# Kernel optimization log

Measured on AMD Instinct MI355X. Metric: run time of the kernel, lower is better.

Reference implementation:

```python
import jax, jax.numpy as jnp
import numpy as np

B, S, D = 32, 4096, 256


def setup_inputs() -> dict:
    key = jax.random.key(0)
    kx, km = jax.random.split(key)
    x = jax.random.normal(kx, (B, S, D), dtype=jnp.float32)
    # keep_mask[b, t] == 1 means timestep t is kept (original: 1 - bernoulli(skipping_probs))
    keep_mask = jax.random.randint(km, (B, S), 0, 2, dtype=jnp.int32)
    return {"x": x, "keep_mask": keep_mask}


def reference(x, keep_mask):
    # Batched stream-compaction: move kept timesteps to the front of each row
    # (stable, preserving original order), zero-pad the tail.
    keep = keep_mask.astype(bool)                       # [B, S]
    # stable argsort of (not keep): kept indices first, in original time order
    order = jnp.argsort(jnp.logical_not(keep), axis=1, stable=True)  # [B, S]
    gathered = jnp.take_along_axis(x, order[:, :, None], axis=1)      # [B, S, D]
    counts = jnp.sum(keep, axis=1, keepdims=True)       # [B, 1] kept lengths
    valid = jnp.arange(S)[None, :] < counts             # [B, S]
    return gathered * valid[:, :, None].astype(x.dtype)
```

## Files before the change

kernel.cpp:

```cpp
#include <hip/hip_runtime.h>

constexpr int S_LEN = 4096;
constexpr int D_DIM = 256;

__global__ void scan_kernel(const int* __restrict__ mask,
                            int* __restrict__ pos,
                            int* __restrict__ counts) {
    const int b = blockIdx.x;
    __shared__ int wsum[8];
    const int tid = threadIdx.x;
    const int base = b * S_LEN + tid * 8;

    int4 m0 = *reinterpret_cast<const int4*>(mask + base);
    int4 m1 = *reinterpret_cast<const int4*>(mask + base + 4);
    int vals[8] = {m0.x, m0.y, m0.z, m0.w, m1.x, m1.y, m1.z, m1.w};

    int local = 0;
#pragma unroll
    for (int i = 0; i < 8; ++i) local += vals[i];

    const int lane = tid & 63;
    const int wid  = tid >> 6;

    int scan = local;
#pragma unroll
    for (int off = 1; off < 64; off <<= 1) {
        int n = __shfl_up(scan, off, 64);
        if (lane >= off) scan += n;
    }
    if (lane == 63) wsum[wid] = scan;
    __syncthreads();

    if (tid == 0) {
        int acc = 0;
#pragma unroll
        for (int i = 0; i < 8; ++i) { int t = wsum[i]; wsum[i] = acc; acc += t; }
        counts[b] = acc;
    }
    __syncthreads();

    int excl = wsum[wid] + (scan - local);
#pragma unroll
    for (int i = 0; i < 8; ++i) {
        pos[base + i] = excl;
        excl += vals[i];
    }
}

__global__ void scatter_kernel(const float* __restrict__ x,
                               const int* __restrict__ mask,
                               const int* __restrict__ pos,
                               const int* __restrict__ counts,
                               float* __restrict__ out) {
    const int wave_in_block = threadIdx.x >> 6;
    const int lane = threadIdx.x & 63;
    const int row  = blockIdx.x * 4 + wave_in_block;
    const int b = row >> 12;
    const int t = row & (S_LEN - 1);

    const int keep = mask[b * S_LEN + t];
    const int p    = pos[b * S_LEN + t];
    const int cnt  = counts[b];
    const int orow = keep ? p : (cnt + (t - p));

    const size_t in_off  = ((size_t)b * S_LEN + t)    * D_DIM;
    const size_t out_off = ((size_t)b * S_LEN + orow) * D_DIM;

    float4 v;
    if (keep) {
        v = reinterpret_cast<const float4*>(x + in_off)[lane];
    } else {
        v = make_float4(0.f, 0.f, 0.f, 0.f);
    }
    reinterpret_cast<float4*>(out + out_off)[lane] = v;
}

extern "C" void kernel_launch(void* const* d_in, const int* in_sizes, int n_in,
                              void* d_out, int out_size, void* d_ws, size_t ws_size,
                              hipStream_t stream) {
    const float* x    = (const float*)d_in[0];
    const int*   mask = (const int*)d_in[1];
    float*       out  = (float*)d_out;

    const int B = in_sizes[1] / S_LEN;

    int* pos    = (int*)d_ws;
    int* counts = pos + (size_t)B * S_LEN;

    scan_kernel<<<B, 512, 0, stream>>>(mask, pos, counts);

    const int rows = B * S_LEN;
    scatter_kernel<<<rows / 4, 256, 0, stream>>>(x, mask, pos, counts, out);
}
```

Before: 221.2 us.

## Fuse prefix-scan and scatter into one kernel with per-block redundant scan

Replaces the separate scan and scatter kernels with a single kernel in which each block recomputes the full-row mask prefix sum in shared memory and then moves its 16 rows. This removes the second launch and the global pos/counts round trip. In exchange, every block redundantly reads the whole mask row and performs a block-wide scan with syncs, which adds L2 traffic and latency before the data copy starts.

```diff
diff --git a/kernel.cpp b/kernel.cpp
--- a/kernel.cpp
+++ b/kernel.cpp
@@ -2,77 +2,72 @@
 
 constexpr int S_LEN = 4096;
 constexpr int D_DIM = 256;
+constexpr int ROWS_PER_BLOCK = 16;
+constexpr int BLOCK_THREADS  = ROWS_PER_BLOCK * 64;
+constexpr int BLOCKS_PER_BATCH = S_LEN / ROWS_PER_BLOCK;
 
-__global__ void scan_kernel(const int* __restrict__ mask,
-                            int* __restrict__ pos,
-                            int* __restrict__ counts) {
-    const int b = blockIdx.x;
-    __shared__ int wsum[8];
-    const int tid = threadIdx.x;
-    const int base = b * S_LEN + tid * 8;
+__global__ __launch_bounds__(BLOCK_THREADS)
+void fused_compact_kernel(const float* __restrict__ x,
+                          const int* __restrict__ mask,
+                          float* __restrict__ out) {
+    const int b   = blockIdx.x / BLOCKS_PER_BATCH;
+    const int blk = blockIdx.x % BLOCKS_PER_BATCH;
+    const int t0  = blk * ROWS_PER_BLOCK;
 
-    int4 m0 = *reinterpret_cast<const int4*>(mask + base);
-    int4 m1 = *reinterpret_cast<const int4*>(mask + base + 4);
-    int vals[8] = {m0.x, m0.y, m0.z, m0.w, m1.x, m1.y, m1.z, m1.w};
+    __shared__ int wtot[16];
+    __shared__ int spos[ROWS_PER_BLOCK];
+    __shared__ int skeep[ROWS_PER_BLOCK];
 
-    int local = 0;
-#pragma unroll
-    for (int i = 0; i < 8; ++i) local += vals[i];
-
+    const int tid  = threadIdx.x;
     const int lane = tid & 63;
     const int wid  = tid >> 6;
 
-    int scan = local;
+    const int e0 = tid * 4;
+    int4 m = *reinterpret_cast<const int4*>(mask + b * S_LEN + e0);
+    int v[4] = {m.x, m.y, m.z, m.w};
+    const int tot = v[0] + v[1] + v[2] + v[3];
+
+    int scan = tot;
 #pragma unroll
     for (int off = 1; off < 64; off <<= 1) {
         int n = __shfl_up(scan, off, 64);
         if (lane >= off) scan += n;
     }
-    if (lane == 63) wsum[wid] = scan;
+    if (lane == 63) wtot[wid] = scan;
     __syncthreads();
 
-    if (tid == 0) {
-        int acc = 0;
+    int wexcl = 0, cnt = 0;
 #pragma unroll
-        for (int i = 0; i < 8; ++i) { int t = wsum[i]; wsum[i] = acc; acc += t; }
-        counts[b] = acc;
+    for (int i = 0; i < 16; ++i) {
+        int w = wtot[i];
+        if (i < wid) wexcl += w;
+        cnt += w;
+    }
+
+    int excl = wexcl + (scan - tot);
+
+#pragma unroll
+    for (int i = 0; i < 4; ++i) {
+        int r = (e0 + i) - t0;
+        if ((unsigned)r < (unsigned)ROWS_PER_BLOCK) {
+            spos[r]  = excl;
+            skeep[r] = v[i];
+        }
+        excl += v[i];
     }
     __syncthreads();
 
-    int excl = wsum[wid] + (scan - local);
-#pragma unroll
-    for (int i = 0; i < 8; ++i) {
-        pos[base + i] = excl;
-        excl += vals[i];
-    }
-}
-
-__global__ void scatter_kernel(const float* __restrict__ x,
-                               const int* __restrict__ mask,
-                               const int* __restrict__ pos,
-                               const int* __restrict__ counts,
-                               float* __restrict__ out) {
-    const int wave_in_block = threadIdx.x >> 6;
-    const int lane = threadIdx.x & 63;
-    const int row  = blockIdx.x * 4 + wave_in_block;
-    const int b = row >> 12;
-    const int t = row & (S_LEN - 1);
-
-    const int keep = mask[b * S_LEN + t];
-    const int p    = pos[b * S_LEN + t];
-    const int cnt  = counts[b];
+    const int t    = t0 + wid;
+    const int keep = skeep[wid];
+    const int p    = spos[wid];
     const int orow = keep ? p : (cnt + (t - p));
 
     const size_t in_off  = ((size_t)b * S_LEN + t)    * D_DIM;
     const size_t out_off = ((size_t)b * S_LEN + orow) * D_DIM;
 
-    float4 v;
-    if (keep) {
-        v = reinterpret_cast<const float4*>(x + in_off)[lane];
-    } else {
-        v = make_float4(0.f, 0.f, 0.f, 0.f);
-    }
-    reinterpret_cast<float4*>(out + out_off)[lane] = v;
+    float4 val = make_float4(0.f, 0.f, 0.f, 0.f);
+    if (keep) val = reinterpret_cast<const float4*>(x + in_off)[lane];
+    reinterpret_cast<float4*>(out + out_off)[lane] = val;
 }
 
 extern "C" void kernel_launch(void* const* d_in, const int* in_sizes, int n_in,
@@ -83,12 +78,7 @@
     float*       out  = (float*)d_out;
 
     const int B = in_sizes[1] / S_LEN;
+    const int grid = B * BLOCKS_PER_BATCH;
 
-    int* pos    = (int*)d_ws;
-    int* counts = pos + (size_t)B * S_LEN;
-
-    scan_kernel<<<B, 512, 0, stream>>>(mask, pos, counts);
-
-    const int rows = B * S_LEN;
-    scatter_kernel<<<rows / 4, 256, 0, stream>>>(x, mask, pos, counts, out);
+    fused_compact_kernel<<<grid, BLOCK_THREADS, 0, stream>>>(x, mask, out);
 }
```

Result: slower. 232.3 us (+5.0%).
